# Kernel tuning notes

Measured on AMD Instinct MI355X. Metric: run time of the kernel, lower is better.

The kernel has to match this reference:

```python
import jax, jax.numpy as jnp
import numpy as np

N_LAYERS, H, D, DFF, V = 6, 16, 1024, 4096, 512
B, S = 4, 2048
DK = D // H
EPS = 1e-6
NEG = -1000000000.0


def _pe_table(max_len, d):
    pos = np.arange(max_len, dtype=np.float32)[:, None]
    div = 1.0 / (10000.0 ** (np.arange(0, d, 2, dtype=np.float32) / d))
    pe = np.zeros((max_len, d), dtype=np.float32)
    pe[:, 0::2] = np.sin(pos * div)
    pe[:, 1::2] = np.cos(pos * div)
    return jnp.asarray(pe[None])  # [1, max_len, d]


def setup_inputs() -> dict:
    key = jax.random.key(0)
    ks = jax.random.split(key, 20)
    f = lambda k, shp: (jax.random.normal(k, shp, dtype=jnp.float32) * 0.02)
    inp = {
        "tgt": jax.random.randint(ks[0], (B, S), 0, V, dtype=jnp.int64),
        "tgt_mask": jnp.tril(jnp.ones((S, S), dtype=jnp.int32))[None],  # [1,S,S] causal
        "emb": f(ks[1], (V, D)),
        "pe": _pe_table(S, D),
        "Wq": f(ks[2], (N_LAYERS, H, D, DK)), "bq": f(ks[3], (N_LAYERS, H, DK)),
        "Wk": f(ks[4], (N_LAYERS, H, D, DK)), "bk": f(ks[5], (N_LAYERS, H, DK)),
        "Wv": f(ks[6], (N_LAYERS, H, D, DK)), "bv": f(ks[7], (N_LAYERS, H, DK)),
        "Wo": f(ks[8], (N_LAYERS, D, D)), "bo": f(ks[9], (N_LAYERS, D)),
        "W1": f(ks[10], (N_LAYERS, D, DFF)), "b1": f(ks[11], (N_LAYERS, DFF)),
        "W2": f(ks[12], (N_LAYERS, DFF, D)), "b2": f(ks[13], (N_LAYERS, D)),
        "ln1_a": jnp.ones((N_LAYERS, D)), "ln1_b": jnp.zeros((N_LAYERS, D)),
        "ln2_a": jnp.ones((N_LAYERS, D)), "ln2_b": jnp.zeros((N_LAYERS, D)),
        "lnf_a": jnp.ones((D,)), "lnf_b": jnp.zeros((D,)),
    }
    return inp


def _ln(x, a, b):
    # torch: a*(x-mean)/(std+eps)+b with unbiased std
    m = x.mean(-1, keepdims=True)
    var = ((x - m) ** 2).sum(-1, keepdims=True) / (x.shape[-1] - 1)
    return a * (x - m) / (jnp.sqrt(var) + EPS) + b


def reference(tgt, tgt_mask, emb, pe, Wq, bq, Wk, bk, Wv, bv, Wo, bo,
              W1, b1, W2, b2, ln1_a, ln1_b, ln2_a, ln2_b, lnf_a, lnf_b):
    d = emb.shape[1]
    s = tgt.shape[1]
    x = emb[tgt] * jnp.sqrt(jnp.float32(d)) + pe[:, :s]  # [B,S,D]
    dk = Wq.shape[-1]
    scale = jnp.sqrt(jnp.float32(dk))

    def layer(x, p):
        wq, bq_, wk, bk_, wv, bv_, wo, bo_, w1, b1_, w2, b2_, a1, g1, a2, g2 = p
        h = _ln(x, a1, g1)
        q = jnp.einsum('bsd,hdk->bhsk', h, wq) + bq_[:, None, :]
        k = jnp.einsum('bsd,hdk->bhsk', h, wk) + bk_[:, None, :]
        v = jnp.einsum('bsd,hdk->bhsk', h, wv) + bv_[:, None, :]
        sc = jnp.einsum('bhsk,bhtk->bhst', q, k) / scale
        sc = jnp.where(tgt_mask[:, None] == 0, jnp.float32(NEG), sc)
        att = jax.nn.softmax(sc, axis=-1)
        o = jnp.einsum('bhst,bhtk->bhsk', att, v)
        o = o.transpose(0, 2, 1, 3).reshape(x.shape)  # concat heads (head order)
        x = x + (o @ wo + bo_)
        h2 = _ln(x, a2, g2)
        x = x + (jnp.maximum(h2 @ w1 + b1_, 0.0) @ w2 + b2_)
        return x, None

    x, _ = jax.lax.scan(layer, x, (Wq, bq, Wk, bk, Wv, bv, Wo, bo,
                                   W1, b1, W2, b2, ln1_a, ln1_b, ln2_a, ln2_b))
    return _ln(x, lnf_a, lnf_b)
```

## Files before the change

### kernel.cpp

```cpp
#include <hip/hip_runtime.h>

typedef __bf16 bf16;
typedef float f32x4 __attribute__((ext_vector_type(4)));
typedef __bf16 bf16x8 __attribute__((ext_vector_type(8)));
typedef __bf16 bf16x4 __attribute__((ext_vector_type(4)));
typedef __bf16 bf16x2 __attribute__((ext_vector_type(2)));

#define NL 6
#define NH 16
#define DM 1024
#define DFF 4096
#define SEQ 2048
#define NB 4
#define NTOK (NB*SEQ)

__device__ __forceinline__ void gload16(const void* g, void* l) {
  __builtin_amdgcn_global_load_lds((const __attribute__((address_space(1))) void*)g,
                                   (__attribute__((address_space(3))) void*)l, 16, 0, 0);
}

__global__ __launch_bounds__(256) void repack_t(const float* __restrict__ src,
                                                bf16* __restrict__ out, int K, int N) {
  const int l = blockIdx.z;
  const int d0 = blockIdx.x * 32, n0 = blockIdx.y * 32;
  __shared__ float t[32][33];
  const int tx = threadIdx.x & 31, ty = threadIdx.x >> 5;
  const float* s = src + (size_t)l * K * N;
  #pragma unroll
  for (int j = 0; j < 4; ++j)
    t[ty*4 + j][tx] = s[(size_t)(d0 + ty*4 + j) * N + n0 + tx];
  __syncthreads();
  bf16* o = out + (size_t)l * N * K;
  #pragma unroll
  for (int j = 0; j < 4; ++j)
    o[(size_t)(n0 + ty*4 + j) * K + d0 + tx] = (bf16)t[tx][ty*4 + j];
}

__global__ __launch_bounds__(256) void repack_qkv(const float* __restrict__ Wq,
                                                  const float* __restrict__ Wk,
                                                  const float* __restrict__ Wv,
                                                  bf16* __restrict__ out) {
  const int l = blockIdx.z;
  const int d0 = blockIdx.x * 32, n0 = blockIdx.y * 32;
  __shared__ float t[32][33];
  const int tx = threadIdx.x & 31, ty = threadIdx.x >> 5;
  const int which = n0 >> 10, h = (n0 & 1023) >> 6, kh0 = n0 & 63;
  const float* W = (which == 0) ? Wq : (which == 1 ? Wk : Wv);
  const float* s = W + ((size_t)(l*NH + h) * DM) * 64 + kh0;
  #pragma unroll
  for (int j = 0; j < 4; ++j)
    t[ty*4 + j][tx] = s[(size_t)(d0 + ty*4 + j) * 64 + tx];
  __syncthreads();
  bf16* o = out + (size_t)l * 3072 * DM + (size_t)n0 * DM + d0;
  #pragma unroll
  for (int j = 0; j < 4; ++j)
    o[(size_t)(ty*4 + j) * DM + tx] = (bf16)t[tx][ty*4 + j];
}

__global__ __launch_bounds__(256) void repack_b(const float* __restrict__ bq,
                                                const float* __restrict__ bk,
                                                const float* __restrict__ bv,
                                                float* __restrict__ out) {
  const int i = blockIdx.x * 256 + threadIdx.x;
  if (i >= NL * 3072) return;
  const int l = i / 3072, n = i % 3072;
  const int which = n >> 10, h = (n >> 6) & 15, kh = n & 63;
  const float* b = (which == 0) ? bq : (which == 1 ? bk : bv);
  out[i] = b[(l*NH + h) * 64 + kh];
}

__global__ __launch_bounds__(256) void embed_k(const int* __restrict__ tgt,
                                               const float* __restrict__ emb,
                                               const float* __restrict__ pe,
                                               float* __restrict__ x) {
  const int i = blockIdx.x;
  const int spos = i & (SEQ - 1);
  const int tok = tgt[i];
  const int tid = threadIdx.x;
  float4 e = ((const float4*)(emb + (size_t)tok * DM))[tid];
  float4 p = ((const float4*)(pe + (size_t)spos * DM))[tid];
  float4 r; r.x = e.x*32.f + p.x; r.y = e.y*32.f + p.y; r.z = e.z*32.f + p.z; r.w = e.w*32.f + p.w;
  ((float4*)(x + (size_t)i * DM))[tid] = r;
}

template<bool OB>
__global__ __launch_bounds__(256) void ln_k(const float* __restrict__ x,
                                            const float* __restrict__ a,
                                            const float* __restrict__ bsh,
                                            bf16* __restrict__ ob, float* __restrict__ of) {
  __shared__ float red[8];
  const int row = blockIdx.x, tid = threadIdx.x;
  const float4 v = ((const float4*)(x + (size_t)row * DM))[tid];
  float s = v.x + v.y + v.z + v.w;
  #pragma unroll
  for (int off = 32; off > 0; off >>= 1) s += __shfl_down(s, off);
  if ((tid & 63) == 0) red[tid >> 6] = s;
  __syncthreads();
  const float mean = (red[0] + red[1] + red[2] + red[3]) * (1.f / 1024.f);
  const float d0 = v.x - mean, d1 = v.y - mean, d2 = v.z - mean, d3 = v.w - mean;
  float ss = d0*d0 + d1*d1 + d2*d2 + d3*d3;
  #pragma unroll
  for (int off = 32; off > 0; off >>= 1) ss += __shfl_down(ss, off);
  if ((tid & 63) == 0) red[4 + (tid >> 6)] = ss;
  __syncthreads();
  const float var = (red[4] + red[5] + red[6] + red[7]) * (1.f / 1023.f);
  const float inv = 1.f / (sqrtf(var) + 1e-6f);
  const float4 av = ((const float4*)a)[tid];
  const float4 bv = ((const float4*)bsh)[tid];
  const float r0 = av.x * d0 * inv + bv.x;
  const float r1 = av.y * d1 * inv + bv.y;
  const float r2 = av.z * d2 * inv + bv.z;
  const float r3 = av.w * d3 * inv + bv.w;
  if (OB) {
    bf16x4 w; w[0] = (bf16)r0; w[1] = (bf16)r1; w[2] = (bf16)r2; w[3] = (bf16)r3;
    ((bf16x4*)(ob + (size_t)row * DM))[tid] = w;
  } else {
    float4 w; w.x = r0; w.y = r1; w.z = r2; w.w = r3;
    ((float4*)(of + (size_t)row * DM))[tid] = w;
  }
}

#define BARRIER() asm volatile("s_barrier" ::: "memory")
#define VMW(n)    asm volatile("s_waitcnt vmcnt(" #n ")" ::: "memory")

template<int EPI>
__global__ __launch_bounds__(512, 1) void gemm8(const bf16* __restrict__ A,
                                                const bf16* __restrict__ B,
                                                const float* __restrict__ bias,
                                                float* __restrict__ xres,
                                                bf16* __restrict__ outb,
                                                bf16* __restrict__ vtb,
                                                int K, int ldc, int Klen) {
  __shared__ __align__(16) char lds[131072];
  const int tid = threadIdx.x;
  const int m0 = blockIdx.x * 256, n0 = blockIdx.y * 256;
  A += (size_t)blockIdx.z * Klen;
  B += (size_t)blockIdx.z * Klen;
  const int wid = tid >> 6, lane = tid & 63;
  const int wm = wid >> 2, wn = wid & 3;
  const int fr = lane & 15, fq = lane >> 4;
  const int fl16 = (fq * 16 + fr) * 16;
  const int s0 = tid, s1 = tid + 512;
  const int r0 = ((s0 >> 7) << 4) | (s0 & 15), c0 = (((s0 >> 6) & 1) << 2) | ((s0 >> 4) & 3);
  const int r1 = ((s1 >> 7) << 4) | (s1 & 15), c1 = (((s1 >> 6) & 1) << 2) | ((s1 >> 4) & 3);
  const bf16* Ap0 = A + (size_t)(m0 + r0) * K + c0 * 8;
  const bf16* Ap1 = A + (size_t)(m0 + r1) * K + c1 * 8;
  const bf16* Bp0 = B + (size_t)(n0 + r0) * K + c0 * 8;
  const bf16* Bp1 = B + (size_t)(n0 + r1) * K + c1 * 8;
  const size_t rskip = (size_t)128 * K;
  const int aRd = wm * 16384;
  const int bRd = 32768 + (wn >> 1) * 16384;
  const int bN = (wn & 1) * 4;

  f32x4 acc[8][4] = {};
  bf16x8 af8[8][2], bfr[4][2];

#define ST_A(d, h, kt) { \
  gload16(Ap0 + (size_t)(h) * rskip + (kt), lds + (d)*65536 + (h)*16384 + s0*16); \
  gload16(Ap1 + (size_t)(h) * rskip + (kt), lds + (d)*65536 + (h)*16384 + s1*16); }
#define ST_B(d, h, kt) { \
  gload16(Bp0 + (size_t)(h) * rskip + (kt), lds + (d)*65536 + 32768 + (h)*16384 + s0*16); \
  gload16(Bp1 + (size_t)(h) * rskip + (kt), lds + (d)*65536 + 32768 + (h)*16384 + s1*16); }
#define LD_A(d, mb) { _Pragma("unroll") for (int m_ = 0; m_ < 4; ++m_) \
    _Pragma("unroll") for (int ks_ = 0; ks_ < 2; ++ks_) \
      af8[(mb) + m_][ks_] = *(const bf16x8*)(lds + (d)*65536 + aRd + ((mb) + m_)*2048 + ks_*1024 + fl16); }
#define LD_B(d, nb) { _Pragma("unroll") for (int n_ = 0; n_ < 2; ++n_) \
    _Pragma("unroll") for (int ks_ = 0; ks_ < 2; ++ks_) \
      bfr[(nb) + n_][ks_] = *(const bf16x8*)(lds + (d)*65536 + bRd + (bN + (nb) + n_)*2048 + ks_*1024 + fl16); }
#define MFMA_Q(mb, nb) { __builtin_amdgcn_s_setprio(1); \
  _Pragma("unroll") for (int m_ = 0; m_ < 4; ++m_) \
  _Pragma("unroll") for (int n_ = 0; n_ < 2; ++n_) \
  _Pragma("unroll") for (int ks_ = 0; ks_ < 2; ++ks_) \
    acc[(mb) + m_][(nb) + n_] = __builtin_amdgcn_mfma_f32_16x16x32_bf16( \
        af8[(mb) + m_][ks_], bfr[(nb) + n_][ks_], acc[(mb) + m_][(nb) + n_], 0, 0, 0); \
  __builtin_amdgcn_s_setprio(0); }

  ST_A(0, 0, 0); ST_A(0, 1, 0);
  ST_B(0, 0, 0); ST_B(0, 1, 0);
  ST_A(1, 0, 64); ST_A(1, 1, 64);
  VMW(4);
  BARRIER();

  const int niter = Klen >> 7;
  for (int it = 0; it < niter; ++it) {
    const int ktB1 = (2 * it + 1) << 6;
    const int ktE2 = (2 * it + 2) << 6;
    const int ktO3 = (2 * it + 3) << 6;
    const bool more = (it + 1 < niter);
    LD_A(0, 0); LD_B(0, 0);
    ST_B(1, 0, ktB1);
    BARRIER(); MFMA_Q(0, 0); BARRIER();
    LD_A(0, 4);
    ST_B(1, 1, ktB1);
    BARRIER(); MFMA_Q(4, 0); BARRIER();
    LD_B(0, 2);
    if (more) ST_A(0, 0, ktE2);
    BARRIER(); MFMA_Q(4, 2); BARRIER();
    if (more) { ST_A(0, 1, ktE2); VMW(4); } else { VMW(0); }
    BARRIER(); MFMA_Q(0, 2); BARRIER();
    LD_A(1, 0); LD_B(1, 0);
    if (more) ST_B(0, 0, ktE2);
    BARRIER(); MFMA_Q(0, 0); BARRIER();
    LD_A(1, 4);
    if (more) ST_B(0, 1, ktE2);
    BARRIER(); MFMA_Q(4, 0); BARRIER();
    LD_B(1, 2);
    if (more) ST_A(1, 0, ktO3);
    BARRIER(); MFMA_Q(4, 2); BARRIER();
    if (more) { ST_A(1, 1, ktO3); VMW(4); }
    BARRIER(); MFMA_Q(0, 2); BARRIER();
  }
#undef ST_A
#undef ST_B
#undef LD_A
#undef LD_B
#undef MFMA_Q

  const float zf = (blockIdx.z == 0) ? 1.f : 0.f;
  #pragma unroll
  for (int m = 0; m < 8; ++m) {
    const int row = m0 + wm * 128 + m * 16 + fq * 4;
    #pragma unroll
    for (int n = 0; n < 4; ++n) {
      const int col = n0 + wn * 64 + n * 16 + fr;
      float bc = bias[col];
      if constexpr (EPI == 4) bc *= zf;
      if constexpr (EPI == 3) {
        if (col >= 2048) {
          const int hh = (col - 2048) >> 6, dkk = col & 63;
          const int bb = row >> 11, tt = row & 2047;
          bf16x4 w;
          #pragma unroll
          for (int j = 0; j < 4; ++j) w[j] = (bf16)(acc[m][n][j] + bc);
          *(bf16x4*)(vtb + ((((size_t)bb*NH + hh)*64 + dkk)*SEQ + tt)) = w;
          continue;
        }
      }
      #pragma unroll
      for (int j = 0; j < 4; ++j) {
        const float v = acc[m][n][j] + bc;
        if constexpr (EPI == 4) {
          atomicAdd(xres + (size_t)(row + j) * ldc + col, v);
        } else if constexpr (EPI == 1) {
          xres[(size_t)(row + j) * ldc + col] += v;
        } else if constexpr (EPI == 2) {
          outb[(size_t)(row + j) * ldc + col] = (bf16)fmaxf(v, 0.f);
        } else {
          outb[(size_t)(row + j) * ldc + col] = (bf16)v;
        }
      }
    }
  }
}

template<int EPI>
__global__ __launch_bounds__(512, 1) void gemm8n(const bf16* __restrict__ A,
                                                 const bf16* __restrict__ B,
                                                 const float* __restrict__ bias,
                                                 float* __restrict__ xres,
                                                 bf16* __restrict__ outb,
                                                 bf16* __restrict__ vtb,
                                                 int K, int ldc) {
  __shared__ __align__(16) char lds[131072];
  const int tid = threadIdx.x;
  const int m0 = blockIdx.x * 128, n0 = blockIdx.y * 256;
  const int wid = tid >> 6, lane = tid & 63;
  const int wm = wid >> 2, wn = wid & 3;
  const int fr = lane & 15, fq = lane >> 4;
  const int fl16 = (fq * 16 + fr) * 16;
  const int s0 = tid, s1 = tid + 512;
  const int r0 = ((s0 >> 7) << 4) | (s0 & 15), c0 = (((s0 >> 6) & 1) << 2) | ((s0 >> 4) & 3);
  const int r1 = ((s1 >> 7) << 4) | (s1 & 15), c1 = (((s1 >> 6) & 1) << 2) | ((s1 >> 4) & 3);
  const bf16* Ap0 = A + (size_t)(m0 + r0) * K + c0 * 8;
  const bf16* Ap1 = A + (size_t)(m0 + r1) * K + c1 * 8;
  const bf16* Bp0 = B + (size_t)(n0 + r0) * K + c0 * 8;
  const bf16* Bp1 = B + (size_t)(n0 + r1) * K + c1 * 8;
  const size_t rskipB = (size_t)128 * K;
  const int aRd = wm * 8192;
  const int bRd = wn * 8192;

  f32x4 acc[4][4] = {};
  bf16x8 af[4][2], bfr[4][2];

#define ST_An(d, kt) { \
  gload16(Ap0 + (kt), lds + (d)*16384 + s0*16); \
  gload16(Ap1 + (kt), lds + (d)*16384 + s1*16); }
#define ST_Bn(j, h, kt) { \
  gload16(Bp0 + (size_t)(h) * rskipB + (kt), lds + 32768 + (j)*32768 + (h)*16384 + s0*16); \
  gload16(Bp1 + (size_t)(h) * rskipB + (kt), lds + 32768 + (j)*32768 + (h)*16384 + s1*16); }
#define LD_An(d) { _Pragma("unroll") for (int m_ = 0; m_ < 4; ++m_) \
    _Pragma("unroll") for (int ks_ = 0; ks_ < 2; ++ks_) \
      af[m_][ks_] = *(const bf16x8*)(lds + (d)*16384 + aRd + m_*2048 + ks_*1024 + fl16); }
#define LD_Bn(j, nb) { _Pragma("unroll") for (int n_ = 0; n_ < 2; ++n_) \
    _Pragma("unroll") for (int ks_ = 0; ks_ < 2; ++ks_) \
      bfr[(nb) + n_][ks_] = *(const bf16x8*)(lds + 32768 + (j)*32768 + bRd + ((nb) + n_)*2048 + ks_*1024 + fl16); }
#define MFMA_H(nb) { __builtin_amdgcn_s_setprio(1); \
  _Pragma("unroll") for (int m_ = 0; m_ < 4; ++m_) \
  _Pragma("unroll") for (int n_ = 0; n_ < 2; ++n_) \
  _Pragma("unroll") for (int ks_ = 0; ks_ < 2; ++ks_) \
    acc[m_][(nb) + n_] = __builtin_amdgcn_mfma_f32_16x16x32_bf16( \
        af[m_][ks_], bfr[(nb) + n_][ks_], acc[m_][(nb) + n_], 0, 0, 0); \
  __builtin_amdgcn_s_setprio(0); }

  ST_An(0, 0);
  ST_Bn(0, 0, 0); ST_Bn(0, 1, 0);
  ST_An(1, 64);
  ST_Bn(1, 0, 64); ST_Bn(1, 1, 64);
  VMW(0);
  BARRIER();

  const int nt = K >> 6;
  int j = 0;
  for (int t = 0; t < nt; ++t) {
    const int d = t & 1;
    const int j2 = (j + 2 >= 3) ? (j - 1) : (j + 2);
    const bool more = (t + 2 < nt);
    const int kt2 = (t + 2) << 6;
    LD_An(d); LD_Bn(j, 0);
    if (more) { ST_Bn(j2, 0, kt2); ST_Bn(j2, 1, kt2); }
    BARRIER(); MFMA_H(0); BARRIER();
    LD_Bn(j, 2);
    if (more) { ST_An(d, kt2); VMW(6); } else { VMW(0); }
    BARRIER(); MFMA_H(2); BARRIER();
    j = (j + 1 >= 3) ? 0 : (j + 1);
  }
#undef ST_An
#undef ST_Bn
#undef LD_An
#undef LD_Bn
#undef MFMA_H

  #pragma unroll
  for (int m = 0; m < 4; ++m) {
    const int row = m0 + wm * 64 + m * 16 + fq * 4;
    #pragma unroll
    for (int n = 0; n < 4; ++n) {
      const int col = n0 + wn * 64 + n * 16 + fr;
      const float bc = bias[col];
      if constexpr (EPI == 3) {
        if (col >= 2048) {
          const int hh = (col - 2048) >> 6, dkk = col & 63;
          const int bb = row >> 11, tt = row & 2047;
          bf16x4 w;
          #pragma unroll
          for (int jj = 0; jj < 4; ++jj) w[jj] = (bf16)(acc[m][n][jj] + bc);
          *(bf16x4*)(vtb + ((((size_t)bb*NH + hh)*64 + dkk)*SEQ + tt)) = w;
          continue;
        }
      }
      #pragma unroll
      for (int jj = 0; jj < 4; ++jj) {
        const float v = acc[m][n][jj] + bc;
        if constexpr (EPI == 1) {
          xres[(size_t)(row + jj) * ldc + col] += v;
        } else if constexpr (EPI == 2) {
          outb[(size_t)(row + jj) * ldc + col] = (bf16)fmaxf(v, 0.f);
        } else {
          outb[(size_t)(row + jj) * ldc + col] = (bf16)v;
        }
      }
    }
  }
}

__global__ __launch_bounds__(256) void attn5_k(const bf16* __restrict__ qk,
                                               const bf16* __restrict__ vt,
                                               bf16* __restrict__ o) {
  __shared__ __align__(16) bf16 Ks[64 * 64];
  __shared__ __align__(16) bf16 Vs[64 * 64];
  __shared__ __align__(16) bf16 Ps[4][16 * 64];
  const int flat = blockIdx.y * 16 + blockIdx.x;
  const int xcd = flat & 7, slot = flat >> 3;
  const int bh = xcd * 8 + (slot >> 4);
  const int pairi = slot & 15;
  const int b = bh >> 4, h = bh & 15;
  const int tid = threadIdx.x;
  const int wave = tid >> 6, lane = tid & 63;
  const int fr = lane & 15, fq = lane >> 4;
  const bf16* Qg = qk + (size_t)b * SEQ * 2048 + h * 64;
  const bf16* Kg = Qg + 1024;
  const bf16* Vtg = vt + (size_t)bh * 64 * SEQ;
  char* Ksc = (char*)Ks;
  char* Vsc = (char*)Vs;
  char* Pw = (char*)&Ps[wave][0];
  const int fr7 = fr & 7;

  for (int pass = 0; pass < 2; ++pass) {
    const int qb = (pass == 0) ? pairi : (31 - pairi);
    const int q0w = qb * 64 + wave * 16;
    const int qrow = q0w + fr;
    const bf16x8 qf0 = *(const bf16x8*)(Qg + (size_t)qrow * 2048 + fq * 8);
    const bf16x8 qf1 = *(const bf16x8*)(Qg + (size_t)qrow * 2048 + 32 + fq * 8);
    f32x4 oacc[4] = {};
    float mrun = -1e30f, lrun = 0.f;
    const int nt = qb + 1;
    for (int kt = 0; kt < nt; ++kt) {
      const int t0 = kt * 64;
      __syncthreads();
      #pragma unroll
      for (int s2 = 0; s2 < 2; ++s2) {
        const int slot2 = tid + s2 * 256;
        const int r = slot2 >> 3, mm = slot2 & 7;
        const int gc = (mm ^ (r & 7)) * 8;
        gload16(Kg + (size_t)(t0 + r) * 2048 + gc, Ksc + slot2 * 16);
        gload16(Vtg + (size_t)r * SEQ + t0 + gc, Vsc + slot2 * 16);
      }
      __syncthreads();
      if (t0 > q0w + 15) continue;
      f32x4 s[4] = {};
      #pragma unroll
      for (int n = 0; n < 4; ++n) {
        const int t_ = n * 16 + fr;
        const bf16x8 k0 = *(const bf16x8*)(Ksc + (t_ * 8 + (fq ^ (t_ & 7))) * 16);
        const bf16x8 k1 = *(const bf16x8*)(Ksc + (t_ * 8 + ((fq + 4) ^ (t_ & 7))) * 16);
        s[n] = __builtin_amdgcn_mfma_f32_16x16x32_bf16(k0, qf0, s[n], 0, 0, 0);
        s[n] = __builtin_amdgcn_mfma_f32_16x16x32_bf16(k1, qf1, s[n], 0, 0, 0);
      }
      float sv[16];
      #pragma unroll
      for (int n = 0; n < 4; ++n)
        #pragma unroll
        for (int jj = 0; jj < 4; ++jj)
          sv[n * 4 + jj] = s[n][jj] * 0.125f;
      const bool need_mask = (t0 + 63 > q0w);
      if (need_mask) {
        #pragma unroll
        for (int i = 0; i < 16; ++i) {
          const int t_abs = t0 + (i >> 2) * 16 + fq * 4 + (i & 3);
          if (t_abs > qrow) sv[i] = -1e30f;
        }
      }
      float a8[8];
      #pragma unroll
      for (int i = 0; i < 8; ++i) a8[i] = fmaxf(sv[i], sv[i + 8]);
      float a4[4];
      #pragma unroll
      for (int i = 0; i < 4; ++i) a4[i] = fmaxf(a8[i], a8[i + 4]);
      float mt = fmaxf(fmaxf(a4[0], a4[1]), fmaxf(a4[2], a4[3]));
      mt = fmaxf(mt, __shfl_xor(mt, 16));
      mt = fmaxf(mt, __shfl_xor(mt, 32));
      const float mnew = fmaxf(mrun, mt);
      const float corr = __expf(mrun - mnew);
      mrun = mnew;
      #pragma unroll
      for (int i = 0; i < 16; ++i) sv[i] = __expf(sv[i] - mnew);
      #pragma unroll
      for (int i = 0; i < 8; ++i) a8[i] = sv[i] + sv[i + 8];
      #pragma unroll
      for (int i = 0; i < 4; ++i) a4[i] = a8[i] + a8[i + 4];
      float ps = (a4[0] + a4[1]) + (a4[2] + a4[3]);
      ps += __shfl_xor(ps, 16);
      ps += __shfl_xor(ps, 32);
      lrun = lrun * corr + ps;
      float cv[4];
      #pragma unroll
      for (int jj = 0; jj < 4; ++jj) cv[jj] = __shfl(corr, fq * 4 + jj);
      #pragma unroll
      for (int nd = 0; nd < 4; ++nd)
        #pragma unroll
        for (int jj = 0; jj < 4; ++jj)
          oacc[nd][jj] *= cv[jj];
      #pragma unroll
      for (int n = 0; n < 4; ++n)
        #pragma unroll
        for (int jp = 0; jp < 2; ++jp) {
          bf16x2 w; w[0] = (bf16)sv[n * 4 + jp * 2]; w[1] = (bf16)sv[n * 4 + jp * 2 + 1];
          const int byteoff = n * 32 + fq * 8 + jp * 4;
          const int chunk = byteoff >> 4, within = byteoff & 15;
          *(bf16x2*)(Pw + fr * 128 + ((chunk ^ fr7) << 4) + within) = w;
        }
      #pragma unroll
      for (int ks = 0; ks < 2; ++ks) {
        const bf16x8 pa = *(const bf16x8*)(Pw + fr * 128 + (((ks * 4 + fq) ^ fr7) << 4));
        #pragma unroll
        for (int nd = 0; nd < 4; ++nd) {
          const int dk_ = nd * 16 + fr;
          const bf16x8 vf = *(const bf16x8*)(Vsc + (dk_ * 8 + ((ks * 4 + fq) ^ (dk_ & 7))) * 16);
          oacc[nd] = __builtin_amdgcn_mfma_f32_16x16x32_bf16(pa, vf, oacc[nd], 0, 0, 0);
        }
      }
    }
    float lv[4];
    #pragma unroll
    for (int jj = 0; jj < 4; ++jj) lv[jj] = __shfl(lrun, fq * 4 + jj);
    #pragma unroll
    for (int nd = 0; nd < 4; ++nd) {
      const int col = h * 64 + nd * 16 + fr;
      #pragma unroll
      for (int jj = 0; jj < 4; ++jj) {
        const int row = q0w + fq * 4 + jj;
        o[((size_t)b * SEQ + row) * DM + col] = (bf16)(oacc[nd][jj] / lv[jj]);
      }
    }
  }
}

extern "C" void kernel_launch(void* const* d_in, const int* in_sizes, int n_in,
                              void* d_out, int out_size, void* d_ws, size_t ws_size,
                              hipStream_t stream) {
  const int*   tgt  = (const int*)d_in[0];
  const float* emb  = (const float*)d_in[2];
  const float* pe   = (const float*)d_in[3];
  const float* Wq   = (const float*)d_in[4];
  const float* bq   = (const float*)d_in[5];
  const float* Wk   = (const float*)d_in[6];
  const float* bk   = (const float*)d_in[7];
  const float* Wv   = (const float*)d_in[8];
  const float* bv   = (const float*)d_in[9];
  const float* Wo   = (const float*)d_in[10];
  const float* bo   = (const float*)d_in[11];
  const float* W1   = (const float*)d_in[12];
  const float* b1   = (const float*)d_in[13];
  const float* W2   = (const float*)d_in[14];
  const float* b2   = (const float*)d_in[15];
  const float* ln1a = (const float*)d_in[16];
  const float* ln1b = (const float*)d_in[17];
  const float* ln2a = (const float*)d_in[18];
  const float* ln2b = (const float*)d_in[19];
  const float* lnfa = (const float*)d_in[20];
  const float* lnfb = (const float*)d_in[21];

  char* ws = (char*)d_ws;
  size_t off = 0;
  bf16*  wqkv = (bf16*)(ws + off);  off += (size_t)NL * 3072 * DM * 2;
  bf16*  wo_  = (bf16*)(ws + off);  off += (size_t)NL * DM * DM * 2;
  bf16*  w1_  = (bf16*)(ws + off);  off += (size_t)NL * DFF * DM * 2;
  bf16*  w2_  = (bf16*)(ws + off);  off += (size_t)NL * DM * DFF * 2;
  float* bqkv = (float*)(ws + off); off += (size_t)NL * 3072 * 4;
  float* x    = (float*)(ws + off); off += (size_t)NTOK * DM * 4;
  bf16*  hbuf = (bf16*)(ws + off);  off += (size_t)NTOK * DM * 2;
  bf16*  qkb  = (bf16*)(ws + off);  off += (size_t)NTOK * 2048 * 2;
  bf16*  vtb  = (bf16*)(ws + off);  off += (size_t)NB * NH * 64 * SEQ * 2;
  bf16*  obuf = (bf16*)(ws + off);  off += (size_t)NTOK * DM * 2;
  bf16*  ubuf = qkb;

  repack_qkv<<<dim3(32, 96, NL), 256, 0, stream>>>(Wq, Wk, Wv, wqkv);
  repack_t  <<<dim3(32, 32, NL), 256, 0, stream>>>(Wo, wo_, DM, DM);
  repack_t  <<<dim3(32, 128, NL), 256, 0, stream>>>(W1, w1_, DM, DFF);
  repack_t  <<<dim3(128, 32, NL), 256, 0, stream>>>(W2, w2_, DFF, DM);
  repack_b  <<<72, 256, 0, stream>>>(bq, bk, bv, bqkv);
  embed_k   <<<NTOK, 256, 0, stream>>>(tgt, emb, pe, x);

  for (int l = 0; l < NL; ++l) {
    ln_k<true><<<NTOK, 256, 0, stream>>>(x, ln1a + l * DM, ln1b + l * DM, hbuf, nullptr);
    gemm8n<3><<<dim3(64, 12), 512, 0, stream>>>(hbuf, wqkv + (size_t)l * 3072 * DM,
                                                bqkv + l * 3072, nullptr, qkb, vtb, DM, 2048);
    attn5_k<<<dim3(16, 64), 256, 0, stream>>>(qkb, vtb, obuf);
    gemm8<4><<<dim3(32, 4, 2), 512, 0, stream>>>(obuf, wo_ + (size_t)l * DM * DM,
                                                 bo + l * DM, x, nullptr, nullptr, DM, DM, DM / 2);
    ln_k<true><<<NTOK, 256, 0, stream>>>(x, ln2a + l * DM, ln2b + l * DM, hbuf, nullptr);
    gemm8<2><<<dim3(32, 16), 512, 0, stream>>>(hbuf, w1_ + (size_t)l * DFF * DM,
                                               b1 + l * DFF, nullptr, ubuf, nullptr, DM, DFF, DM);
    gemm8<4><<<dim3(32, 4, 2), 512, 0, stream>>>(ubuf, w2_ + (size_t)l * DM * DFF,
                                                 b2 + l * DM, x, nullptr, nullptr, DFF, DM, DFF / 2);
  }
  ln_k<false><<<NTOK, 256, 0, stream>>>(x, lnfa, lnfb, nullptr, (float*)d_out);

  (void)in_sizes; (void)n_in; (void)out_size; (void)ws_size;
}
```

Before: 2.879 ms.

## Swizzle GEMM blocks across XCDs, fold Q scaling, skip softmax rescale, drop split-K Wo

Adds an XCD-aware block-index remap to both GEMM kernels so neighbouring tiles land on the same chiplet and share L2. Moves the 1/sqrt(dk) scale into the QKV GEMM epilogue for the Q columns, taking a multiply out of the attention inner loop. Skips the online-softmax correction whenever no lane's running max grows. Replaces the split-K atomic Wo GEMM with the non-split gemm8n using a plain residual add, removing atomics at the cost of fewer blocks.

```diff
diff --git a/kernel.cpp b/kernel.cpp
--- a/kernel.cpp
+++ b/kernel.cpp
@@ -17,6 +17,19 @@
 __device__ __forceinline__ void gload16(const void* g, void* l) {
   __builtin_amdgcn_global_load_lds((const __attribute__((address_space(1))) void*)g,
                                    (__attribute__((address_space(3))) void*)l, 16, 0, 0);
+}
+
+struct Bid { int x, y, z; };
+__device__ __forceinline__ Bid swz3() {
+  const int gx = gridDim.x, gy = gridDim.y;
+  const int nwg = gx * gy * gridDim.z;
+  const int orig = blockIdx.x + gx * (blockIdx.y + gy * blockIdx.z);
+  const int xcd = orig & 7, rest = orig >> 3;
+  const int q = nwg >> 3, r = nwg & 7;
+  const int base = (xcd < r) ? xcd * (q + 1) : r * (q + 1) + (xcd - r) * q;
+  const int nid = base + rest;
+  Bid b; b.x = nid % gx; const int rem = nid / gx; b.y = rem % gy; b.z = rem / gy;
+  return b;
 }
 
 __global__ __launch_bounds__(256) void repack_t(const float* __restrict__ src,
@@ -133,9 +146,10 @@
                                                 int K, int ldc, int Klen) {
   __shared__ __align__(16) char lds[131072];
   const int tid = threadIdx.x;
-  const int m0 = blockIdx.x * 256, n0 = blockIdx.y * 256;
-  A += (size_t)blockIdx.z * Klen;
-  B += (size_t)blockIdx.z * Klen;
+  const Bid bidx = swz3();
+  const int m0 = bidx.x * 256, n0 = bidx.y * 256;
+  A += (size_t)bidx.z * Klen;
+  B += (size_t)bidx.z * Klen;
   const int wid = tid >> 6, lane = tid & 63;
   const int wm = wid >> 2, wn = wid & 3;
   const int fr = lane & 15, fq = lane >> 4;
@@ -216,7 +230,7 @@
 #undef LD_B
 #undef MFMA_Q
 
-  const float zf = (blockIdx.z == 0) ? 1.f : 0.f;
+  const float zf = (bidx.z == 0) ? 1.f : 0.f;
   #pragma unroll
   for (int m = 0; m < 8; ++m) {
     const int row = m0 + wm * 128 + m * 16 + fq * 4;
@@ -238,7 +252,8 @@
       }
       #pragma unroll
       for (int j = 0; j < 4; ++j) {
-        const float v = acc[m][n][j] + bc;
+        float v = acc[m][n][j] + bc;
+        if constexpr (EPI == 3) { if (col < 1024) v *= 0.125f; }
         if constexpr (EPI == 4) {
           atomicAdd(xres + (size_t)(row + j) * ldc + col, v);
         } else if constexpr (EPI == 1) {
@@ -263,7 +278,8 @@
                                                  int K, int ldc) {
   __shared__ __align__(16) char lds[131072];
   const int tid = threadIdx.x;
-  const int m0 = blockIdx.x * 128, n0 = blockIdx.y * 256;
+  const Bid bidx = swz3();
+  const int m0 = bidx.x * 128, n0 = bidx.y * 256;
   const int wid = tid >> 6, lane = tid & 63;
   const int wm = wid >> 2, wn = wid & 3;
   const int fr = lane & 15, fq = lane >> 4;
@@ -350,7 +366,8 @@
       }
       #pragma unroll
       for (int jj = 0; jj < 4; ++jj) {
-        const float v = acc[m][n][jj] + bc;
+        float v = acc[m][n][jj] + bc;
+        if constexpr (EPI == 3) { if (col < 1024) v *= 0.125f; }
         if constexpr (EPI == 1) {
           xres[(size_t)(row + jj) * ldc + col] += v;
         } else if constexpr (EPI == 2) {
@@ -421,7 +438,7 @@
       for (int n = 0; n < 4; ++n)
         #pragma unroll
         for (int jj = 0; jj < 4; ++jj)
-          sv[n * 4 + jj] = s[n][jj] * 0.125f;
+          sv[n * 4 + jj] = s[n][jj];
       const bool need_mask = (t0 + 63 > q0w);
       if (need_mask) {
         #pragma unroll
@@ -439,8 +456,10 @@
       float mt = fmaxf(fmaxf(a4[0], a4[1]), fmaxf(a4[2], a4[3]));
       mt = fmaxf(mt, __shfl_xor(mt, 16));
       mt = fmaxf(mt, __shfl_xor(mt, 32));
+      const bool grow = __any(mt > mrun);
       const float mnew = fmaxf(mrun, mt);
-      const float corr = __expf(mrun - mnew);
+      float corr = 1.f;
+      if (grow) corr = __expf(mrun - mnew);
       mrun = mnew;
       #pragma unroll
       for (int i = 0; i < 16; ++i) sv[i] = __expf(sv[i] - mnew);
@@ -451,15 +470,19 @@
       float ps = (a4[0] + a4[1]) + (a4[2] + a4[3]);
       ps += __shfl_xor(ps, 16);
       ps += __shfl_xor(ps, 32);
-      lrun = lrun * corr + ps;
-      float cv[4];
-      #pragma unroll
-      for (int jj = 0; jj < 4; ++jj) cv[jj] = __shfl(corr, fq * 4 + jj);
-      #pragma unroll
-      for (int nd = 0; nd < 4; ++nd)
+      if (grow) {
+        lrun = lrun * corr + ps;
+        float cv[4];
         #pragma unroll
-        for (int jj = 0; jj < 4; ++jj)
-          oacc[nd][jj] *= cv[jj];
+        for (int jj = 0; jj < 4; ++jj) cv[jj] = __shfl(corr, fq * 4 + jj);
+        #pragma unroll
+        for (int nd = 0; nd < 4; ++nd)
+          #pragma unroll
+          for (int jj = 0; jj < 4; ++jj)
+            oacc[nd][jj] *= cv[jj];
+      } else {
+        lrun += ps;
+      }
       #pragma unroll
       for (int n = 0; n < 4; ++n)
         #pragma unroll
@@ -546,8 +569,8 @@
     gemm8n<3><<<dim3(64, 12), 512, 0, stream>>>(hbuf, wqkv + (size_t)l * 3072 * DM,
                                                 bqkv + l * 3072, nullptr, qkb, vtb, DM, 2048);
     attn5_k<<<dim3(16, 64), 256, 0, stream>>>(qkb, vtb, obuf);
-    gemm8<4><<<dim3(32, 4, 2), 512, 0, stream>>>(obuf, wo_ + (size_t)l * DM * DM,
-                                                 bo + l * DM, x, nullptr, nullptr, DM, DM, DM / 2);
+    gemm8n<1><<<dim3(64, 4), 512, 0, stream>>>(obuf, wo_ + (size_t)l * DM * DM,
+                                               bo + l * DM, x, nullptr, nullptr, DM, DM);
     ln_k<true><<<NTOK, 256, 0, stream>>>(x, ln2a + l * DM, ln2b + l * DM, hbuf, nullptr);
     gemm8<2><<<dim3(32, 16), 512, 0, stream>>>(hbuf, w1_ + (size_t)l * DFF * DM,
                                                b1 + l * DFF, nullptr, ubuf, nullptr, DM, DFF, DM);
```

Measured after the change: 2.726 ms. 5.3% less time.
